# Performance work log

Measured on AMD Instinct MI355X. Metric: run time of the kernel, lower is better.

The kernel has to match this reference:

```python
import jax, jax.numpy as jnp
import numpy as np

LN_EPS = 1e-5


def setup_inputs() -> dict:
    key = jax.random.key(0)
    k1, k2, k3, k4 = jax.random.split(key, 4)
    N, C, E = 100000, 128, 1600000
    x = jax.random.normal(k1, (N, C), dtype=jnp.float32)
    edge_index = jax.random.randint(k2, (2, E), 0, N, dtype=jnp.int64)
    gamma = jnp.ones((C,), dtype=jnp.float32)
    beta = jnp.zeros((C,), dtype=jnp.float32)
    scale = 1.0 / np.sqrt(C)
    W_l = jax.random.normal(k3, (C, C), dtype=jnp.float32) * scale
    b_l = jnp.zeros((C,), dtype=jnp.float32)
    W_r = jax.random.normal(k4, (C, C), dtype=jnp.float32) * scale
    return {"x": x, "edge_index": edge_index, "gamma": gamma, "beta": beta,
            "W_l": W_l, "b_l": b_l, "W_r": W_r}


def reference(x, edge_index, gamma, beta, W_l, b_l, W_r):
    # Pre-norm residual block: LayerNorm -> ReLU -> SAGEConv(mean) -> (dropout=identity in eval) -> +x
    N = x.shape[0]
    # LayerNorm over channels
    mu = jnp.mean(x, axis=-1, keepdims=True)
    var = jnp.mean(jnp.square(x - mu), axis=-1, keepdims=True)
    h = (x - mu) * jax.lax.rsqrt(var + LN_EPS) * gamma + beta
    h = jax.nn.relu(h)
    # SAGEConv with mean aggregation (PyG default):
    # out = lin_l(mean_{j in N(i)} h_j) + lin_r(h_i)
    src, dst = edge_index[0], edge_index[1]
    msgs = h[src]                                               # [E, C] gather
    agg = jax.ops.segment_sum(msgs, dst, num_segments=N)        # [N, C]
    cnt = jax.ops.segment_sum(jnp.ones((src.shape[0],), dtype=h.dtype), dst,
                              num_segments=N)                   # [N]
    mean = jnp.where(cnt[:, None] > 0, agg / jnp.maximum(cnt[:, None], 1.0), 0.0)
    out = mean @ W_l.T + b_l + h @ W_r.T
    return out + x
```

## Files before the change

### kernel.cpp

```cpp
#include <hip/hip_runtime.h>

typedef __attribute__((ext_vector_type(8))) short short8;
typedef __attribute__((ext_vector_type(4))) float float4v;

#define P1B   256
#define GS    64
#define GSH   6
#define AGS   32
#define ELCAP 768
#define GCAP  2048

__device__ __forceinline__ unsigned short f2bf(float f) {
    union { float f; unsigned u; } v; v.f = f;
    unsigned r = v.u + 0x7fffu + ((v.u >> 16) & 1u);
    return (unsigned short)(r >> 16);
}
__device__ __forceinline__ float bf2f(unsigned short u) {
    union { unsigned u; float f; } v; v.u = ((unsigned)u) << 16; return v.f;
}

__global__ __launch_bounds__(256) void fused_pre_kernel(
    const float* __restrict__ x, const float* __restrict__ gamma,
    const float* __restrict__ beta, unsigned* __restrict__ hbuf,
    const int* __restrict__ idx, int* __restrict__ gdeg,
    const float* __restrict__ Wl, const float* __restrict__ Wr,
    unsigned short* __restrict__ wsb, int N, int E, int LNB, int G) {
    const int b = blockIdx.x, t = threadIdx.x;
    if (b < P1B) {
        __shared__ int hist[GCAP];
        for (int i = t; i < G; i += 256) hist[i] = 0;
        __syncthreads();
        const int CH = (E + P1B - 1) / P1B;
        const int e0 = b * CH, e1 = min(E, e0 + CH);
        for (int e = e0 + t; e < e1; e += 256)
            atomicAdd(&hist[idx[E + e] >> GSH], 1);
        __syncthreads();
        for (int i = t; i < G; i += 256)
            if (hist[i]) atomicAdd(&gdeg[i], hist[i]);
    } else if (b < P1B + LNB) {
        const int row = (b - P1B) * 4 + (t >> 6);
        if (row >= N) return;
        const int lane = t & 63;
        const size_t base = (size_t)row * 128 + lane * 2;
        float2 v = *(const float2*)&x[base];
        float s = v.x + v.y;
        #pragma unroll
        for (int o = 32; o; o >>= 1) s += __shfl_xor(s, o, 64);
        const float mu = s * 0.0078125f;
        const float d0 = v.x - mu, d1 = v.y - mu;
        float ss = d0 * d0 + d1 * d1;
        #pragma unroll
        for (int o = 32; o; o >>= 1) ss += __shfl_xor(ss, o, 64);
        const float rs = rsqrtf(ss * 0.0078125f + 1e-5f);
        float2 g = *(const float2*)&gamma[lane * 2];
        float2 bb = *(const float2*)&beta[lane * 2];
        float h0 = fmaxf(fmaf(d0 * rs, g.x, bb.x), 0.f);
        float h1 = fmaxf(fmaf(d1 * rs, g.y, bb.y), 0.f);
        hbuf[(size_t)row * 64 + lane] = (unsigned)f2bf(h0) | ((unsigned)f2bf(h1) << 16);
    } else {
        const int s = (b - P1B - LNB) * 256 + t;
        const int tc = s >> 9, c = (s >> 6) & 7, l = s & 63;
        const int n  = tc * 16 + (l & 15);
        const int k0 = c * 32 + ((l >> 4) & 3) * 8;
        const float* w = (k0 < 128) ? (Wl + (size_t)n * 128 + k0)
                                    : (Wr + (size_t)n * 128 + (k0 - 128));
        unsigned short tmp[8];
        #pragma unroll
        for (int j = 0; j < 8; j++) tmp[j] = f2bf(w[j]);
        *(short8*)&wsb[(size_t)s * 8] = *(short8*)tmp;
    }
}

__global__ __launch_bounds__(1024) void gscan_kernel(
    const int* __restrict__ gdeg, int* __restrict__ gstart,
    int* __restrict__ gcur, int G) {
    __shared__ int sd[1024];
    const int t = threadIdx.x;
    const int i0 = 2 * t, i1 = 2 * t + 1;
    const int v0 = (i0 < G) ? gdeg[i0] : 0;
    const int v1 = (i1 < G) ? gdeg[i1] : 0;
    const int pr = v0 + v1;
    sd[t] = pr;
    __syncthreads();
    for (int off = 1; off < 1024; off <<= 1) {
        int u = (t >= off) ? sd[t - off] : 0;
        __syncthreads();
        sd[t] += u;
        __syncthreads();
    }
    const int ex = sd[t] - pr;
    if (i0 <= G) { gstart[i0] = ex;      if (i0 < G) gcur[i0] = ex; }
    if (i1 <= G) { gstart[i1] = ex + v0; if (i1 < G) gcur[i1] = ex + v0; }
}

__global__ __launch_bounds__(1024) void bucketize_kernel(
    const int* __restrict__ idx, int* __restrict__ gcur,
    int* __restrict__ gbuf, int E, int G) {
    __shared__ int hist[GCAP], base[GCAP];
    const int t = threadIdx.x, b = blockIdx.x;
    for (int i = t; i < G; i += 1024) hist[i] = 0;
    __syncthreads();
    const int CH = (E + P1B - 1) / P1B;
    const int e0 = b * CH, e1 = min(E, e0 + CH);
    for (int e = e0 + t; e < e1; e += 1024)
        atomicAdd(&hist[idx[E + e] >> GSH], 1);
    __syncthreads();
    for (int i = t; i < G; i += 1024) {
        const int c = hist[i];
        base[i] = c ? atomicAdd(&gcur[i], c) : 0;
        hist[i] = 0;
    }
    __syncthreads();
    for (int e = e0 + t; e < e1; e += 1024) {
        const int dst = idx[E + e];
        const int src = idx[e];
        const int g = dst >> GSH;
        const int pos = base[g] + atomicAdd(&hist[g], 1);
        gbuf[pos] = (src << GSH) | (dst & (GS - 1));
    }
}

__global__ __launch_bounds__(256) void aggregate_kernel(
    const unsigned* __restrict__ hbuf, const int* __restrict__ gbuf,
    const int* __restrict__ gstart, unsigned* __restrict__ mbuf, int N) {
    __shared__ int elds[ELCAP];
    __shared__ int hist[AGS], segstart[AGS], cur[AGS];
    const int t = threadIdx.x, w = t >> 6, l = t & 63;
    const int b = blockIdx.x;
    const int g = b >> 1, half = b & 1;
    const int n0 = b << 5;
    const int e0 = gstart[g], cnt = gstart[g + 1] - e0;

    if (t < AGS) hist[t] = 0;
    __syncthreads();
    for (int i = t; i < cnt; i += 256) {
        const int r = gbuf[e0 + i] & (GS - 1);
        if ((r >> 5) == half) atomicAdd(&hist[r & (AGS - 1)], 1);
    }
    __syncthreads();
    if (t < AGS) cur[t] = hist[t];
    __syncthreads();
    for (int off = 1; off < AGS; off <<= 1) {
        int u = (t < AGS && t >= off) ? cur[t - off] : 0;
        __syncthreads();
        if (t < AGS) cur[t] += u;
        __syncthreads();
    }
    if (t < AGS) { segstart[t] = cur[t] - hist[t]; cur[t] = segstart[t]; }
    __syncthreads();
    for (int i = t; i < cnt; i += 256) {
        const int pk = gbuf[e0 + i];
        const int r = pk & (GS - 1);
        if ((r >> 5) == half) {
            const int pos = atomicAdd(&cur[r & (AGS - 1)], 1);
            if (pos < ELCAP) elds[pos] = pk >> GSH;
        }
    }
    __syncthreads();

    for (int i = 0; i < 8; i++) {
        const int ln = w * 8 + i;
        const int node = n0 + ln;
        const int sp = segstart[ln];
        int dend = sp + hist[ln];
        if (dend > ELCAP) dend = ELCAP;
        float a0 = 0.f, a1 = 0.f;
        int j = sp;
        for (; j + 16 <= dend; j += 16) {
            unsigned p[16];
            #pragma unroll
            for (int k = 0; k < 16; k++)
                p[k] = hbuf[(size_t)elds[j + k] * 64 + l];
            #pragma unroll
            for (int k = 0; k < 16; k++) {
                a0 += bf2f((unsigned short)(p[k] & 0xffffu));
                a1 += bf2f((unsigned short)(p[k] >> 16));
            }
        }
        if (j + 8 <= dend) {
            unsigned p[8];
            #pragma unroll
            for (int k = 0; k < 8; k++)
                p[k] = hbuf[(size_t)elds[j + k] * 64 + l];
            #pragma unroll
            for (int k = 0; k < 8; k++) {
                a0 += bf2f((unsigned short)(p[k] & 0xffffu));
                a1 += bf2f((unsigned short)(p[k] >> 16));
            }
            j += 8;
        }
        for (; j < dend; j++) {
            unsigned p = hbuf[(size_t)elds[j] * 64 + l];
            a0 += bf2f((unsigned short)(p & 0xffffu));
            a1 += bf2f((unsigned short)(p >> 16));
        }
        const int dv = hist[ln];
        const float inv = (dv > 0) ? 1.f / (float)dv : 0.f;
        if (node < N)
            mbuf[(size_t)node * 64 + l] =
                (unsigned)f2bf(a0 * inv) | ((unsigned)f2bf(a1 * inv) << 16);
    }
}

__global__ __launch_bounds__(256) void mm_kernel(
    float* __restrict__ out, const unsigned* __restrict__ hbuf,
    const unsigned* __restrict__ mbuf, const float* __restrict__ x,
    const unsigned short* __restrict__ wsb, const float* __restrict__ bl, int N) {
    const int t = threadIdx.x, w = t >> 6, l = t & 63;
    const int rowbase = blockIdx.x * 64 + w * 16;
    if (rowbase >= N) return;
    const int r = l & 15, q = l >> 4;
    const int arow = min(rowbase + r, N - 1);
    const unsigned short* mp = (const unsigned short*)mbuf + (size_t)arow * 128 + q * 8;
    const unsigned short* hp = (const unsigned short*)hbuf + (size_t)arow * 128 + q * 8;
    short8 af[8];
    #pragma unroll
    for (int c = 0; c < 4; c++) af[c]     = *(const short8*)(mp + c * 32);
    #pragma unroll
    for (int c = 0; c < 4; c++) af[4 + c] = *(const short8*)(hp + c * 32);
    #pragma unroll
    for (int cc = 0; cc < 8; cc++) {
        float4v acc = {0.f, 0.f, 0.f, 0.f};
        const short8* bw = (const short8*)wsb + (size_t)cc * 512;
        #pragma unroll
        for (int c = 0; c < 8; c++)
            acc = __builtin_amdgcn_mfma_f32_16x16x32_bf16(af[c], bw[c * 64 + l], acc, 0, 0, 0);
        const int col = cc * 16 + r;
        const float blv = bl[col];
        #pragma unroll
        for (int rr = 0; rr < 4; rr++) {
            const int row = rowbase + q * 4 + rr;
            if (row < N)
                out[(size_t)row * 128 + col] = acc[rr] + blv + x[(size_t)row * 128 + col];
        }
    }
}

extern "C" void kernel_launch(void* const* d_in, const int* in_sizes, int n_in,
                              void* d_out, int out_size, void* d_ws, size_t ws_size,
                              hipStream_t stream) {
    const float* x     = (const float*)d_in[0];
    const int*   ei    = (const int*)d_in[1];
    const float* gamma = (const float*)d_in[2];
    const float* beta  = (const float*)d_in[3];
    const float* Wl    = (const float*)d_in[4];
    const float* bl    = (const float*)d_in[5];
    const float* Wr    = (const float*)d_in[6];
    float* out = (float*)d_out;

    const int C = 128;
    const int N = in_sizes[0] / C;
    const int E = in_sizes[1] / 2;
    const int G = (N + GS - 1) >> GSH;

    char* ws = (char*)d_ws;
    size_t off = 0;
    unsigned* hbuf = (unsigned*)(ws + off); off += (size_t)N * 256;
    unsigned* mbuf = (unsigned*)(ws + off); off += (size_t)N * 256;
    int* gbuf      = (int*)(ws + off);      off += (size_t)E * 4;
    int* gdeg      = (int*)(ws + off);      off += GCAP * 4;
    int* gstart    = (int*)(ws + off);      off += GCAP * 4;
    int* gcur      = (int*)(ws + off);      off += GCAP * 4;
    unsigned short* wsb = (unsigned short*)(ws + off);

    const int LNB = (N + 3) / 4;

    hipMemsetAsync(gdeg, 0, GCAP * 4, stream);
    fused_pre_kernel<<<P1B + LNB + 16, 256, 0, stream>>>(
        x, gamma, beta, hbuf, ei, gdeg, Wl, Wr, wsb, N, E, LNB, G);
    gscan_kernel<<<1, 1024, 0, stream>>>(gdeg, gstart, gcur, G);
    bucketize_kernel<<<P1B, 1024, 0, stream>>>(ei, gcur, gbuf, E, G);
    aggregate_kernel<<<2 * G, 256, 0, stream>>>(hbuf, gbuf, gstart, mbuf, N);
    mm_kernel<<<(N + 63) / 64, 256, 0, stream>>>(out, hbuf, mbuf, x, wsb, bl, N);
}
```

Before: 255.8 us.

## Fuse neighbor-mean aggregation with the MFMA linear layer via LDS

Merges the aggregate and matmul kernels into one. Each block keeps its 32 nodes' bf16 mean vectors in padded shared memory and multiplies them by the packed weights with MFMA right away. This removes the write and re-read of the global mbuf buffer and one kernel launch. In exchange the matmul now runs with 32-row tiles per block, split across four waves by column halves. The padded 16-byte LDS reads may be misaligned for odd rows.

```diff
diff --git a/kernel.cpp b/kernel.cpp
--- a/kernel.cpp
+++ b/kernel.cpp
@@ -9,6 +9,7 @@
 #define AGS   32
 #define ELCAP 768
 #define GCAP  2048
+#define MPAD  66
 
 __device__ __forceinline__ unsigned short f2bf(float f) {
     union { float f; unsigned u; } v; v.f = f;
@@ -120,11 +121,14 @@
     }
 }
 
-__global__ __launch_bounds__(256) void aggregate_kernel(
+__global__ __launch_bounds__(256) void aggmm_kernel(
     const unsigned* __restrict__ hbuf, const int* __restrict__ gbuf,
-    const int* __restrict__ gstart, unsigned* __restrict__ mbuf, int N) {
+    const int* __restrict__ gstart, const unsigned short* __restrict__ wsb,
+    const float* __restrict__ bl, const float* __restrict__ x,
+    float* __restrict__ out, int N) {
     __shared__ int elds[ELCAP];
     __shared__ int hist[AGS], segstart[AGS], cur[AGS];
+    __shared__ unsigned mean_lds[AGS][MPAD];
     const int t = threadIdx.x, w = t >> 6, l = t & 63;
     const int b = blockIdx.x;
     const int g = b >> 1, half = b & 1;
@@ -160,7 +164,6 @@
 
     for (int i = 0; i < 8; i++) {
         const int ln = w * 8 + i;
-        const int node = n0 + ln;
         const int sp = segstart[ln];
         int dend = sp + hist[ln];
         if (dend > ELCAP) dend = ELCAP;
@@ -196,40 +199,35 @@
         }
         const int dv = hist[ln];
         const float inv = (dv > 0) ? 1.f / (float)dv : 0.f;
-        if (node < N)
-            mbuf[(size_t)node * 64 + l] =
-                (unsigned)f2bf(a0 * inv) | ((unsigned)f2bf(a1 * inv) << 16);
-    }
-}
-
-__global__ __launch_bounds__(256) void mm_kernel(
-    float* __restrict__ out, const unsigned* __restrict__ hbuf,
-    const unsigned* __restrict__ mbuf, const float* __restrict__ x,
-    const unsigned short* __restrict__ wsb, const float* __restrict__ bl, int N) {
-    const int t = threadIdx.x, w = t >> 6, l = t & 63;
-    const int rowbase = blockIdx.x * 64 + w * 16;
-    if (rowbase >= N) return;
+        mean_lds[ln][l] = (unsigned)f2bf(a0 * inv) | ((unsigned)f2bf(a1 * inv) << 16);
+    }
+    __syncthreads();
+
+    const int rt = w >> 1, chh = w & 1;
     const int r = l & 15, q = l >> 4;
-    const int arow = min(rowbase + r, N - 1);
-    const unsigned short* mp = (const unsigned short*)mbuf + (size_t)arow * 128 + q * 8;
-    const unsigned short* hp = (const unsigned short*)hbuf + (size_t)arow * 128 + q * 8;
+    const int lrow = rt * 16 + r;
+    const int arow = min(n0 + lrow, N - 1);
     short8 af[8];
     #pragma unroll
-    for (int c = 0; c < 4; c++) af[c]     = *(const short8*)(mp + c * 32);
+    for (int c = 0; c < 4; c++)
+        af[c] = *(const short8*)&mean_lds[lrow][c * 16 + q * 4];
+    const unsigned short* hp = (const unsigned short*)hbuf + (size_t)arow * 128 + q * 8;
     #pragma unroll
-    for (int c = 0; c < 4; c++) af[4 + c] = *(const short8*)(hp + c * 32);
+    for (int c = 0; c < 4; c++)
+        af[4 + c] = *(const short8*)(hp + c * 32);
     #pragma unroll
-    for (int cc = 0; cc < 8; cc++) {
+    for (int cc = 0; cc < 4; cc++) {
+        const int tc = chh * 4 + cc;
         float4v acc = {0.f, 0.f, 0.f, 0.f};
-        const short8* bw = (const short8*)wsb + (size_t)cc * 512;
+        const short8* bw = (const short8*)wsb + (size_t)tc * 512;
         #pragma unroll
         for (int c = 0; c < 8; c++)
             acc = __builtin_amdgcn_mfma_f32_16x16x32_bf16(af[c], bw[c * 64 + l], acc, 0, 0, 0);
-        const int col = cc * 16 + r;
+        const int col = tc * 16 + r;
         const float blv = bl[col];
         #pragma unroll
         for (int rr = 0; rr < 4; rr++) {
-            const int row = rowbase + q * 4 + rr;
+            const int row = n0 + rt * 16 + q * 4 + rr;
             if (row < N)
                 out[(size_t)row * 128 + col] = acc[rr] + blv + x[(size_t)row * 128 + col];
         }
@@ -256,7 +254,6 @@
     char* ws = (char*)d_ws;
     size_t off = 0;
     unsigned* hbuf = (unsigned*)(ws + off); off += (size_t)N * 256;
-    unsigned* mbuf = (unsigned*)(ws + off); off += (size_t)N * 256;
     int* gbuf      = (int*)(ws + off);      off += (size_t)E * 4;
     int* gdeg      = (int*)(ws + off);      off += GCAP * 4;
     int* gstart    = (int*)(ws + off);      off += GCAP * 4;
@@ -270,6 +267,5 @@
         x, gamma, beta, hbuf, ei, gdeg, Wl, Wr, wsb, N, E, LNB, G);
     gscan_kernel<<<1, 1024, 0, stream>>>(gdeg, gstart, gcur, G);
     bucketize_kernel<<<P1B, 1024, 0, stream>>>(ei, gcur, gbuf, E, G);
-    aggregate_kernel<<<2 * G, 256, 0, stream>>>(hbuf, gbuf, gstart, mbuf, N);
-    mm_kernel<<<(N + 63) / 64, 256, 0, stream>>>(out, hbuf, mbuf, x, wsb, bl, N);
-}
+    aggmm_kernel<<<2 * G, 256, 0, stream>>>(hbuf, gbuf, gstart, wsb, bl, x, out, N);
+}
```

Measured after the change: 250.0 us. 2.3% less time.
